# Optimization experiments

Measured on AMD Instinct MI355X. Metric: run time of the kernel, lower is better.

The kernel has to match this reference:

```python
import jax, jax.numpy as jnp
import numpy as np

B, C, H, W = 16384, 1, 2048, 1
HID = 5


def setup_inputs() -> dict:
    key = jax.random.key(0)
    kx, kl, k1, k2, k3, k4 = jax.random.split(key, 6)
    x = jax.random.normal(kx, (B, C, H, W), dtype=jnp.float32)
    # random ragged lengths in [1, H]; zero out padded tail so the module's
    # (x != 0).any(dim=2) mask recovers exactly these lengths
    lengths = jax.random.randint(kl, (B,), 1, H + 1)
    t_idx = jnp.arange(H)
    valid = (t_idx[None, :] < lengths[:, None])  # [B, H]
    x = x * valid[:, None, :, None].astype(jnp.float32)
    s = 1.0 / np.sqrt(HID)
    W_ih = jax.random.uniform(k1, (4 * HID, 1), minval=-s, maxval=s, dtype=jnp.float32)
    W_hh = jax.random.uniform(k2, (4 * HID, HID), minval=-s, maxval=s, dtype=jnp.float32)
    b_ih = jax.random.uniform(k3, (4 * HID,), minval=-s, maxval=s, dtype=jnp.float32)
    b_hh = jax.random.uniform(k4, (4 * HID,), minval=-s, maxval=s, dtype=jnp.float32)
    return {"x": x, "W_ih": W_ih, "W_hh": W_hh, "b_ih": b_ih, "b_hh": b_hh}


def reference(x, W_ih, W_hh, b_ih, b_hh):
    b, c, h, w = x.shape
    feats = c * w  # == 1 (LSTM input_size)
    xr = x.reshape(b, h, feats)  # [B, T, 1]
    mask = jnp.any(xr != 0, axis=2)  # [B, T]
    lengths = mask.sum(axis=1).astype(jnp.int32)  # [B]

    bias = b_ih + b_hh  # [4H]
    # precompute input projection for all timesteps: [B, T, 4H]
    x_proj = jnp.einsum('btf,gf->btg', xr, W_ih) + bias
    xs = jnp.moveaxis(x_proj, 1, 0)  # [T, B, 4H]

    h0 = jnp.zeros((b, HID), dtype=x.dtype)
    c0 = jnp.zeros((b, HID), dtype=x.dtype)

    def step(carry, inp):
        hp, cp = carry
        xg, t = inp
        gates = xg + hp @ W_hh.T  # [B, 4H]
        i, f, g, o = jnp.split(gates, 4, axis=1)
        i = jax.nn.sigmoid(i)
        f = jax.nn.sigmoid(f)
        g = jnp.tanh(g)
        o = jax.nn.sigmoid(o)
        cn = f * cp + i * g
        hn = o * jnp.tanh(cn)
        # packed semantics: only advance state while t < length (per sample)
        upd = (t < lengths)[:, None]
        hn = jnp.where(upd, hn, hp)
        cn = jnp.where(upd, cn, cp)
        return (hn, cn), None

    (hT, cT), _ = jax.lax.scan(step, (h0, c0), (xs, jnp.arange(h)))
    return hT[None]  # [1, B, HID] matching torch h shape
```

## Files before the change

kernel.cpp:

```cpp
#include <hip/hip_runtime.h>

#define Bn   16384
#define Tn   2048
#define HIDn 5

static __device__ __forceinline__ float rcp_fast(float v) {
    return __builtin_amdgcn_rcpf(v);
}
static __device__ __forceinline__ float exp2_fast(float v) {
    return __builtin_amdgcn_exp2f(v);
}

template <int SRC>
static __device__ __forceinline__ float qbcast(float v) {
    constexpr int ctrl = SRC | (SRC << 2) | (SRC << 4) | (SRC << 6);
    return __int_as_float(
        __builtin_amdgcn_update_dpp(0, __float_as_int(v), ctrl, 0xF, 0xF, true));
}

__global__ __launch_bounds__(256) void len_kernel(const float* __restrict__ x,
                                                  int* __restrict__ lengths) {
    const int gtid = blockIdx.x * 256 + threadIdx.x;
    const int row  = gtid >> 6;
    const int lane = threadIdx.x & 63;
    const float4* r = reinterpret_cast<const float4*>(x + (size_t)row * Tn);
    int cnt = 0;
    #pragma unroll
    for (int i = 0; i < Tn / 4 / 64; ++i) {
        float4 v = r[i * 64 + lane];
        cnt += (v.x != 0.0f) + (v.y != 0.0f) + (v.z != 0.0f) + (v.w != 0.0f);
    }
    #pragma unroll
    for (int off = 32; off > 0; off >>= 1) cnt += __shfl_xor(cnt, off, 64);
    if (lane == 0) lengths[row] = cnt;
}

__global__ __launch_bounds__(256) void lstm_kernel(const float* __restrict__ x,
                                                   const float* __restrict__ Wih,
                                                   const float* __restrict__ Whh,
                                                   const float* __restrict__ bih,
                                                   const float* __restrict__ bhh,
                                                   const int* __restrict__ lengths,
                                                   float* __restrict__ out) {
    const int gtid = blockIdx.x * 256 + threadIdx.x;
    const int b = gtid >> 2;
    const int q = gtid & 3;

    const float L2E   = 1.4426950408889634f;
    const float NL2E2 = -2.0f * L2E;

    int   gidx[5] = { q, 5 + q, 10 + q, 15 + q, 5 * q + 4 };
    float sj[5];
    sj[0] = -L2E; sj[1] = -L2E; sj[2] = NL2E2; sj[3] = -L2E;
    sj[4] = (q == 2) ? NL2E2 : -L2E;
    const float mA4 = (q == 2) ? 2.0f : 1.0f;
    const float bA4 = (q == 2) ? -1.0f : 0.0f;

    float wih[5], bias[5], whh[5][5];
    #pragma unroll
    for (int j = 0; j < 5; ++j) {
        const int g = gidx[j];
        wih[j]  = Wih[g] * sj[j];
        bias[j] = (bih[g] + bhh[g]) * sj[j];
        #pragma unroll
        for (int k = 0; k < HIDn; ++k) whh[j][k] = Whh[g * HIDn + k] * sj[j];
    }

    const int len = lengths[b];
    const float* xrow = x + (size_t)b * Tn;

    float h0 = 0, h1 = 0, h2 = 0, h3 = 0, h4 = 0;
    float h_own = 0, cq = 0, c4 = 0;

    int t = 0;
    while (__any(t < len)) {
        const float4 xq = *reinterpret_cast<const float4*>(xrow + t);
        const float xs[4] = { xq.x, xq.y, xq.z, xq.w };

        #pragma unroll
        for (int s = 0; s < 4; ++s) {
            if (t + s < len) {
                const float xv = xs[s];

                float p[5];
                #pragma unroll
                for (int j = 0; j < 5; ++j) {
                    float pp = fmaf(xv, wih[j], bias[j]);
                    pp = fmaf(h0, whh[j][0], pp);
                    pp = fmaf(h1, whh[j][1], pp);
                    pp = fmaf(h2, whh[j][2], pp);
                    pp = fmaf(h3, whh[j][3], pp);
                    pp = fmaf(h4, whh[j][4], pp);
                    p[j] = pp;
                }
                const float r0 = rcp_fast(1.0f + exp2_fast(p[0]));
                const float r1 = rcp_fast(1.0f + exp2_fast(p[1]));
                const float a2 = fmaf(2.0f, rcp_fast(1.0f + exp2_fast(p[2])), -1.0f);
                const float r3 = rcp_fast(1.0f + exp2_fast(p[3]));
                const float a4 = fmaf(mA4, rcp_fast(1.0f + exp2_fast(p[4])), bA4);

                cq = fmaf(r1, cq, r0 * a2);

                const float i4 = qbcast<0>(a4);
                const float f4 = qbcast<1>(a4);
                const float g4 = qbcast<2>(a4);
                const float o4 = qbcast<3>(a4);
                c4 = fmaf(f4, c4, i4 * g4);

                const float thq = fmaf(2.0f, rcp_fast(1.0f + exp2_fast(cq * NL2E2)), -1.0f);
                const float th4 = fmaf(2.0f, rcp_fast(1.0f + exp2_fast(c4 * NL2E2)), -1.0f);
                h_own = r3 * thq;
                h4    = o4 * th4;

                h0 = qbcast<0>(h_own);
                h1 = qbcast<1>(h_own);
                h2 = qbcast<2>(h_own);
                h3 = qbcast<3>(h_own);
            }
        }
        t += 4;
    }

    out[b * HIDn + q] = h_own;
    if (q == 0) out[b * HIDn + 4] = h4;
}

extern "C" void kernel_launch(void* const* d_in, const int* in_sizes, int n_in,
                              void* d_out, int out_size, void* d_ws, size_t ws_size,
                              hipStream_t stream) {
    const float* x   = (const float*)d_in[0];
    const float* Wih = (const float*)d_in[1];
    const float* Whh = (const float*)d_in[2];
    const float* bih = (const float*)d_in[3];
    const float* bhh = (const float*)d_in[4];
    float* out = (float*)d_out;
    int* lengths = (int*)d_ws;

    len_kernel<<<Bn / 4, 256, 0, stream>>>(x, lengths);
    lstm_kernel<<<Bn / 64, 256, 0, stream>>>(x, Wih, Whh, bih, bhh, lengths, out);
}
```

Baseline: 635.3 us.

## Map each batch row to eight lanes with one hidden unit per lane

Moves from four lanes per sample, where one lane redundantly computes the fifth hidden unit, to eight lanes per sample. Each of the first five lanes owns one hidden unit and its four gates, and h is broadcast with ds_swizzle instead of quad DPP. It also prefetches the next float4 of x one iteration ahead, merges two sigmoid reciprocals into one rcp of a product, and adds a launch-bounds occupancy hint. The serial chain per step gets shorter, but the lane count doubles, three of every eight lanes are wasted, and ds_swizzle likely has higher latency than DPP on the critical path.

Result: faster. 610.8 us (-3.8%).

```diff
diff --git a/kernel.cpp b/kernel.cpp
--- a/kernel.cpp
+++ b/kernel.cpp
@@ -11,11 +11,10 @@
     return __builtin_amdgcn_exp2f(v);
 }
 
-template <int SRC>
-static __device__ __forceinline__ float qbcast(float v) {
-    constexpr int ctrl = SRC | (SRC << 2) | (SRC << 4) | (SRC << 6);
+template <int K>
+static __device__ __forceinline__ float bcast8(float v) {
     return __int_as_float(
-        __builtin_amdgcn_update_dpp(0, __float_as_int(v), ctrl, 0xF, 0xF, true));
+        __builtin_amdgcn_ds_swizzle(__float_as_int(v), (K << 5) | 0x18));
 }
 
 __global__ __launch_bounds__(256) void len_kernel(const float* __restrict__ x,
@@ -35,46 +34,42 @@
     if (lane == 0) lengths[row] = cnt;
 }
 
-__global__ __launch_bounds__(256) void lstm_kernel(const float* __restrict__ x,
-                                                   const float* __restrict__ Wih,
-                                                   const float* __restrict__ Whh,
-                                                   const float* __restrict__ bih,
-                                                   const float* __restrict__ bhh,
-                                                   const int* __restrict__ lengths,
-                                                   float* __restrict__ out) {
+__global__ __launch_bounds__(256, 2) void lstm_kernel(const float* __restrict__ x,
+                                                      const float* __restrict__ Wih,
+                                                      const float* __restrict__ Whh,
+                                                      const float* __restrict__ bih,
+                                                      const float* __restrict__ bhh,
+                                                      const int* __restrict__ lengths,
+                                                      float* __restrict__ out) {
     const int gtid = blockIdx.x * 256 + threadIdx.x;
-    const int b = gtid >> 2;
-    const int q = gtid & 3;
+    const int b    = gtid >> 3;
+    const int lsub = threadIdx.x & 7;
+    const int k    = min(lsub, 4);
 
     const float L2E   = 1.4426950408889634f;
     const float NL2E2 = -2.0f * L2E;
 
-    int   gidx[5] = { q, 5 + q, 10 + q, 15 + q, 5 * q + 4 };
-    float sj[5];
-    sj[0] = -L2E; sj[1] = -L2E; sj[2] = NL2E2; sj[3] = -L2E;
-    sj[4] = (q == 2) ? NL2E2 : -L2E;
-    const float mA4 = (q == 2) ? 2.0f : 1.0f;
-    const float bA4 = (q == 2) ? -1.0f : 0.0f;
-
-    float wih[5], bias[5], whh[5][5];
+    float wih[4], bias[4], whh[4][HIDn];
     #pragma unroll
-    for (int j = 0; j < 5; ++j) {
-        const int g = gidx[j];
-        wih[j]  = Wih[g] * sj[j];
-        bias[j] = (bih[g] + bhh[g]) * sj[j];
+    for (int j = 0; j < 4; ++j) {
+        const int   gi = 5 * j + k;
+        const float sj = (j == 2) ? NL2E2 : -L2E;
+        wih[j]  = Wih[gi] * sj;
+        bias[j] = (bih[gi] + bhh[gi]) * sj;
         #pragma unroll
-        for (int k = 0; k < HIDn; ++k) whh[j][k] = Whh[g * HIDn + k] * sj[j];
+        for (int kk = 0; kk < HIDn; ++kk) whh[j][kk] = Whh[gi * HIDn + kk] * sj;
     }
 
     const int len = lengths[b];
     const float* xrow = x + (size_t)b * Tn;
 
     float h0 = 0, h1 = 0, h2 = 0, h3 = 0, h4 = 0;
-    float h_own = 0, cq = 0, c4 = 0;
+    float h_own = 0, c = 0;
 
+    float4 xq = *reinterpret_cast<const float4*>(xrow);
     int t = 0;
     while (__any(t < len)) {
-        const float4 xq = *reinterpret_cast<const float4*>(xrow + t);
+        const float4 xn = *reinterpret_cast<const float4*>(xrow + min(t + 4, Tn - 4));
         const float xs[4] = { xq.x, xq.y, xq.z, xq.w };
 
         #pragma unroll
@@ -82,9 +77,9 @@
             if (t + s < len) {
                 const float xv = xs[s];
 
-                float p[5];
+                float p[4];
                 #pragma unroll
-                for (int j = 0; j < 5; ++j) {
+                for (int j = 0; j < 4; ++j) {
                     float pp = fmaf(xv, wih[j], bias[j]);
                     pp = fmaf(h0, whh[j][0], pp);
                     pp = fmaf(h1, whh[j][1], pp);
@@ -93,36 +88,37 @@
                     pp = fmaf(h4, whh[j][4], pp);
                     p[j] = pp;
                 }
-                const float r0 = rcp_fast(1.0f + exp2_fast(p[0]));
-                const float r1 = rcp_fast(1.0f + exp2_fast(p[1]));
-                const float a2 = fmaf(2.0f, rcp_fast(1.0f + exp2_fast(p[2])), -1.0f);
-                const float r3 = rcp_fast(1.0f + exp2_fast(p[3]));
-                const float a4 = fmaf(mA4, rcp_fast(1.0f + exp2_fast(p[4])), bA4);
+                const float e0 = exp2_fast(p[0]);
+                const float e1 = exp2_fast(p[1]);
+                const float e2 = exp2_fast(p[2]);
+                const float e3 = exp2_fast(p[3]);
+                const float x0 = 1.0f + e0, x1 = 1.0f + e1;
+                const float x2 = 1.0f + e2, x3 = 1.0f + e3;
+                const float r01 = rcp_fast(x0 * x1);
+                const float r23 = rcp_fast(x2 * x3);
+                const float gi_ = x1 * r01;
+                const float gf_ = x0 * r01;
+                const float gg_ = fmaf(2.0f, x3 * r23, -1.0f);
+                const float go_ = x2 * r23;
 
-                cq = fmaf(r1, cq, r0 * a2);
+                c = fmaf(gf_, c, gi_ * gg_);
 
-                const float i4 = qbcast<0>(a4);
-                const float f4 = qbcast<1>(a4);
-                const float g4 = qbcast<2>(a4);
-                const float o4 = qbcast<3>(a4);
-                c4 = fmaf(f4, c4, i4 * g4);
+                const float ec = exp2_fast(c * NL2E2);
+                const float th = fmaf(2.0f, rcp_fast(1.0f + ec), -1.0f);
+                h_own = go_ * th;
 
-                const float thq = fmaf(2.0f, rcp_fast(1.0f + exp2_fast(cq * NL2E2)), -1.0f);
-                const float th4 = fmaf(2.0f, rcp_fast(1.0f + exp2_fast(c4 * NL2E2)), -1.0f);
-                h_own = r3 * thq;
-                h4    = o4 * th4;
-
-                h0 = qbcast<0>(h_own);
-                h1 = qbcast<1>(h_own);
-                h2 = qbcast<2>(h_own);
-                h3 = qbcast<3>(h_own);
+                h0 = bcast8<0>(h_own);
+                h1 = bcast8<1>(h_own);
+                h2 = bcast8<2>(h_own);
+                h3 = bcast8<3>(h_own);
+                h4 = bcast8<4>(h_own);
             }
         }
+        xq = xn;
         t += 4;
     }
 
-    out[b * HIDn + q] = h_own;
-    if (q == 0) out[b * HIDn + 4] = h4;
+    if (lsub < HIDn) out[b * HIDn + lsub] = h_own;
 }
 
 extern "C" void kernel_launch(void* const* d_in, const int* in_sizes, int n_in,
@@ -137,5 +133,5 @@
     int* lengths = (int*)d_ws;
 
     len_kernel<<<Bn / 4, 256, 0, stream>>>(x, lengths);
-    lstm_kernel<<<Bn / 64, 256, 0, stream>>>(x, Wih, Whh, bih, bhh, lengths, out);
+    lstm_kernel<<<Bn * 8 / 256, 256, 0, stream>>>(x, Wih, Whh, bih, bhh, lengths, out);
 }
```
